# Kernel optimization log

Hardware: AMD Instinct MI355X
Metric: run time of the kernel (lower is better)

## Reference

```python
import jax, jax.numpy as jnp
import numpy as np

TEMP = 0.1
DROPOUT_PROB = 0.1
EPS = 1e-8  # torch F.cosine_similarity eps


def setup_inputs() -> dict:
    key = jax.random.key(0)
    k1, k2 = jax.random.split(key)
    N, D = 8192, 1024
    inputs = jax.random.normal(k1, (N, D), dtype=jnp.float32)
    noise = jax.random.uniform(k2, (N, D), dtype=jnp.float32)
    return {"inputs": inputs, "noise": noise}


def reference(inputs, noise):
    keep = 1.0 - DROPOUT_PROB
    # inverted dropout (torch nn.Dropout in train mode)
    mask = jnp.where(noise < keep, 1.0 / keep, 0.0).astype(inputs.dtype)
    enhanced = inputs * mask

    # cosine similarity = normalized matmul; norms clamped at EPS like torch
    na = jnp.maximum(jnp.linalg.norm(inputs, axis=-1, keepdims=True), EPS)
    nb = jnp.maximum(jnp.linalg.norm(enhanced, axis=-1, keepdims=True), EPS)
    a = inputs / na            # (N, D)
    b = enhanced / nb          # (N, D)
    logits = jnp.einsum('nd,md->nm', a, b) / TEMP  # (N, N)

    # cross-entropy with labels = arange(N), mean reduction
    lse = jax.nn.logsumexp(logits, axis=-1)          # (N,)
    diag = jnp.diagonal(logits)                      # (N,)
    return jnp.mean(lse - diag)
```

## Files before the change

kernel.cpp:

```cpp
#include <hip/hip_runtime.h>
#include <hip/hip_bf16.h>

#define N 8192
#define D 1024
#define BM 128
#define BN 256
#define BK 32
#define NKT (D / BK)

static constexpr float TEMP = 0.1f;
static constexpr float KEEP = 0.9f;
static constexpr float EPSN = 1e-8f;

typedef __attribute__((ext_vector_type(8))) short bf16x8;
typedef __attribute__((ext_vector_type(4))) float f32x4;

__device__ __forceinline__ void gload_lds16(const void* gsrc, void* ldst) {
  __builtin_amdgcn_global_load_lds(
      (const __attribute__((address_space(1))) void*)gsrc,
      (__attribute__((address_space(3))) void*)ldst, 16, 0, 0);
}

struct bf4pack { __hip_bfloat16 v[4]; };

__global__ __launch_bounds__(256) void UCR_prep(
    const float* __restrict__ inputs, const float* __restrict__ noise,
    __hip_bfloat16* __restrict__ aB, __hip_bfloat16* __restrict__ bB,
    float* __restrict__ diag, float* __restrict__ S, float* __restrict__ out)
{
  const int row = blockIdx.x;
  const int t = threadIdx.x;
  const float4 x = ((const float4*)(inputs + (size_t)row * D))[t];
  const float4 u = ((const float4*)(noise  + (size_t)row * D))[t];
  const float inv_keep = 1.0f / KEEP;
  float4 e;
  e.x = (u.x < KEEP) ? x.x * inv_keep : 0.0f;
  e.y = (u.y < KEEP) ? x.y * inv_keep : 0.0f;
  e.z = (u.z < KEEP) ? x.z * inv_keep : 0.0f;
  e.w = (u.w < KEEP) ? x.w * inv_keep : 0.0f;

  float sx  = x.x*x.x + x.y*x.y + x.z*x.z + x.w*x.w;
  float se  = e.x*e.x + e.y*e.y + e.z*e.z + e.w*e.w;
  float sxe = x.x*e.x + x.y*e.y + x.z*e.z + x.w*e.w;

  #pragma unroll
  for (int off = 1; off < 64; off <<= 1) {
    sx  += __shfl_xor(sx, off);
    se  += __shfl_xor(se, off);
    sxe += __shfl_xor(sxe, off);
  }
  __shared__ float red[3][4];
  const int wid = t >> 6, lane = t & 63;
  if (lane == 0) { red[0][wid] = sx; red[1][wid] = se; red[2][wid] = sxe; }
  __syncthreads();
  sx  = red[0][0] + red[0][1] + red[0][2] + red[0][3];
  se  = red[1][0] + red[1][1] + red[1][2] + red[1][3];
  sxe = red[2][0] + red[2][1] + red[2][2] + red[2][3];

  const float na = fmaxf(sqrtf(sx), EPSN);
  const float nb = fmaxf(sqrtf(se), EPSN);
  const float sa = 1.0f / (na * TEMP);
  const float sb = 1.0f / nb;
  if (t == 0) {
    diag[row] = sxe / (na * nb * TEMP);
    S[row] = 0.0f;
    if (row == 0) out[0] = 0.0f;
  }

  bf4pack pa, pb;
  pa.v[0] = __float2bfloat16(x.x * sa); pa.v[1] = __float2bfloat16(x.y * sa);
  pa.v[2] = __float2bfloat16(x.z * sa); pa.v[3] = __float2bfloat16(x.w * sa);
  pb.v[0] = __float2bfloat16(e.x * sb); pb.v[1] = __float2bfloat16(e.y * sb);
  pb.v[2] = __float2bfloat16(e.z * sb); pb.v[3] = __float2bfloat16(e.w * sb);
  ((bf4pack*)(aB + (size_t)row * D))[t] = pa;
  ((bf4pack*)(bB + (size_t)row * D))[t] = pb;
}

__global__ __launch_bounds__(256, 2) void UCR_gemm(
    const __hip_bfloat16* __restrict__ Aw, const __hip_bfloat16* __restrict__ Bw,
    float* __restrict__ S)
{
  __shared__ char lds[73728];

  const int t = threadIdx.x;
  const int lane = t & 63;
  const int wid = t >> 6;

  const int bid = blockIdx.x;
  const int u = bid >> 3;
  const int tm = (bid & 7) * 8 + (u & 7);
  const int tn = u >> 3;

  const char* Ag = (const char*)(Aw + (size_t)tm * BM * D);
  const char* Bg = (const char*)(Bw + (size_t)tn * BN * D);

  const char* aS[2]; const char* bS[4]; unsigned xA[2], xB[4];
  #pragma unroll
  for (int j = 0; j < 2; ++j) {
    const unsigned x = (unsigned)t * 16u + (unsigned)j * 4096u;
    const unsigned lin = x ^ (((x >> 7) & 3u) << 4);
    aS[j] = Ag + (size_t)(lin >> 6) * 2048 + (lin & 63u);
    xA[j] = x;
  }
  #pragma unroll
  for (int j = 0; j < 4; ++j) {
    const unsigned x = (unsigned)t * 16u + (unsigned)j * 4096u;
    const unsigned lin = x ^ (((x >> 7) & 3u) << 4);
    bS[j] = Bg + (size_t)(lin >> 6) * 2048 + (lin & 63u);
    xB[j] = x;
  }

#define STAGE(kt, L) do {                                   \
    gload_lds16(aS[0] + (kt) * 64, (L) + xA[0]);            \
    gload_lds16(aS[1] + (kt) * 64, (L) + xA[1]);            \
    gload_lds16(bS[0] + (kt) * 64, (L) + 8192 + xB[0]);     \
    gload_lds16(bS[1] + (kt) * 64, (L) + 8192 + xB[1]);     \
    gload_lds16(bS[2] + (kt) * 64, (L) + 8192 + xB[2]);     \
    gload_lds16(bS[3] + (kt) * 64, (L) + 8192 + xB[3]);     \
  } while (0)

  const int ln = lane & 15;
  const int cq = lane >> 4;
  const int colk = (cq * 16) ^ (((ln >> 1) & 3) << 4);
  const int aoff = ln * 64 + colk;
  const int boff = 8192 + wid * 4096 + ln * 64 + colk;

  f32x4 acc[8][4] = {};

  char* L0 = lds;
  char* L1 = lds + 24576;
  char* L2 = lds + 49152;

  STAGE(0, L0); STAGE(1, L1);
  asm volatile("s_waitcnt vmcnt(6)" ::: "memory");
  __builtin_amdgcn_s_barrier();

  for (int kt = 0; kt < NKT - 2; ++kt) {
    STAGE(kt + 2, L2);
    bf16x8 aF[8], bF[4];
    #pragma unroll
    for (int m = 0; m < 8; ++m)
      aF[m] = *(const bf16x8*)(L0 + m * 1024 + aoff);
    #pragma unroll
    for (int n = 0; n < 4; ++n)
      bF[n] = *(const bf16x8*)(L0 + n * 1024 + boff);
    __builtin_amdgcn_s_setprio(1);
    #pragma unroll
    for (int m = 0; m < 8; ++m)
      #pragma unroll
      for (int n = 0; n < 4; ++n)
        acc[m][n] = __builtin_amdgcn_mfma_f32_16x16x32_bf16(
            aF[m], bF[n], acc[m][n], 0, 0, 0);
    __builtin_amdgcn_s_setprio(0);
    asm volatile("s_waitcnt vmcnt(6)" ::: "memory");
    __builtin_amdgcn_s_barrier();
    char* tmp = L0; L0 = L1; L1 = L2; L2 = tmp;
  }
  {
    bf16x8 aF[8], bF[4];
    #pragma unroll
    for (int m = 0; m < 8; ++m)
      aF[m] = *(const bf16x8*)(L0 + m * 1024 + aoff);
    #pragma unroll
    for (int n = 0; n < 4; ++n)
      bF[n] = *(const bf16x8*)(L0 + n * 1024 + boff);
    __builtin_amdgcn_s_setprio(1);
    #pragma unroll
    for (int m = 0; m < 8; ++m)
      #pragma unroll
      for (int n = 0; n < 4; ++n)
        acc[m][n] = __builtin_amdgcn_mfma_f32_16x16x32_bf16(
            aF[m], bF[n], acc[m][n], 0, 0, 0);
    __builtin_amdgcn_s_setprio(0);
    asm volatile("s_waitcnt vmcnt(0)" ::: "memory");
    __builtin_amdgcn_s_barrier();
    char* tmp = L0; L0 = L1; L1 = L2; L2 = tmp;
  }
  {
    bf16x8 aF[8], bF[4];
    #pragma unroll
    for (int m = 0; m < 8; ++m)
      aF[m] = *(const bf16x8*)(L0 + m * 1024 + aoff);
    #pragma unroll
    for (int n = 0; n < 4; ++n)
      bF[n] = *(const bf16x8*)(L0 + n * 1024 + boff);
    #pragma unroll
    for (int m = 0; m < 8; ++m)
      #pragma unroll
      for (int n = 0; n < 4; ++n)
        acc[m][n] = __builtin_amdgcn_mfma_f32_16x16x32_bf16(
            aF[m], bF[n], acc[m][n], 0, 0, 0);
  }
#undef STAGE

  const int g = lane >> 4;
  const int c = lane & 15;
  const int rowbase = tm * BM;
  #pragma unroll
  for (int m = 0; m < 8; ++m) {
    #pragma unroll
    for (int i = 0; i < 4; ++i) {
      float s = 0.0f;
      #pragma unroll
      for (int n = 0; n < 4; ++n) s += __expf(acc[m][n][i]);
      #pragma unroll
      for (int off = 1; off < 16; off <<= 1) s += __shfl_xor(s, off);
      if (c == 0) atomicAdd(&S[rowbase + m * 16 + g * 4 + i], s);
    }
  }
}

__global__ __launch_bounds__(256) void UCR_loss(
    const float* __restrict__ S, const float* __restrict__ diag,
    float* __restrict__ out)
{
  const int i = blockIdx.x * 256 + threadIdx.x;
  float acc = logf(S[i]) - diag[i];
  #pragma unroll
  for (int off = 1; off < 64; off <<= 1) acc += __shfl_xor(acc, off);
  __shared__ float r[4];
  if ((threadIdx.x & 63) == 0) r[threadIdx.x >> 6] = acc;
  __syncthreads();
  if (threadIdx.x == 0)
    atomicAdd(out, (r[0] + r[1] + r[2] + r[3]) * (1.0f / (float)N));
}

extern "C" void kernel_launch(void* const* d_in, const int* in_sizes, int n_in,
                              void* d_out, int out_size, void* d_ws, size_t ws_size,
                              hipStream_t stream)
{
  const float* inputs = (const float*)d_in[0];
  const float* noise  = (const float*)d_in[1];

  char* ws = (char*)d_ws;
  __hip_bfloat16* aB = (__hip_bfloat16*)ws;
  __hip_bfloat16* bB = aB + (size_t)N * D;
  float* S    = (float*)(bB + (size_t)N * D);
  float* diag = S + N;

  UCR_prep<<<N, 256, 0, stream>>>(inputs, noise, aB, bB, diag, S, (float*)d_out);
  UCR_gemm<<<(N / BM) * (N / BN), 256, 0, stream>>>(aB, bB, S);
  UCR_loss<<<N / 256, 256, 0, stream>>>(S, diag, (float*)d_out);
}
```

Baseline: 246.7 us.

## Switch similarity GEMM from bf16 to scaled fp8 MFMA with exact diagonal

The prep kernel now quantizes the normalized, temperature-scaled operands to fp8 with fixed scale factors of 16 and 64, and the GEMM uses fp8 MFMA instructions with BK doubled to 64. This halves operand bytes and uses the higher-throughput fp8 matrix path. To limit the accuracy loss on the largest logit, diagonal tiles replace the quantized diagonal entry with the fp32 diag value before exponentiation. The risk is fp8 precision error in the logsumexp over the off-diagonal entries.

```diff
diff --git a/kernel.cpp b/kernel.cpp
--- a/kernel.cpp
+++ b/kernel.cpp
@@ -5,14 +5,14 @@
 #define D 1024
 #define BM 128
 #define BN 256
-#define BK 32
+#define BK 64
 #define NKT (D / BK)
 
 static constexpr float TEMP = 0.1f;
 static constexpr float KEEP = 0.9f;
 static constexpr float EPSN = 1e-8f;
-
-typedef __attribute__((ext_vector_type(8))) short bf16x8;
+static constexpr float INVS = 1.0f / 1024.0f;
+
 typedef __attribute__((ext_vector_type(4))) float f32x4;
 
 __device__ __forceinline__ void gload_lds16(const void* gsrc, void* ldst) {
@@ -21,11 +21,9 @@
       (__attribute__((address_space(3))) void*)ldst, 16, 0, 0);
 }
 
-struct bf4pack { __hip_bfloat16 v[4]; };
-
 __global__ __launch_bounds__(256) void UCR_prep(
     const float* __restrict__ inputs, const float* __restrict__ noise,
-    __hip_bfloat16* __restrict__ aB, __hip_bfloat16* __restrict__ bB,
+    unsigned char* __restrict__ a8, unsigned char* __restrict__ b8,
     float* __restrict__ diag, float* __restrict__ S, float* __restrict__ out)
 {
   const int row = blockIdx.x;
@@ -59,26 +57,25 @@
 
   const float na = fmaxf(sqrtf(sx), EPSN);
   const float nb = fmaxf(sqrtf(se), EPSN);
-  const float sa = 1.0f / (na * TEMP);
-  const float sb = 1.0f / nb;
+  const float sa = 16.0f / (na * TEMP);
+  const float sb = 64.0f / nb;
   if (t == 0) {
     diag[row] = sxe / (na * nb * TEMP);
     S[row] = 0.0f;
     if (row == 0) out[0] = 0.0f;
   }
 
-  bf4pack pa, pb;
-  pa.v[0] = __float2bfloat16(x.x * sa); pa.v[1] = __float2bfloat16(x.y * sa);
-  pa.v[2] = __float2bfloat16(x.z * sa); pa.v[3] = __float2bfloat16(x.w * sa);
-  pb.v[0] = __float2bfloat16(e.x * sb); pb.v[1] = __float2bfloat16(e.y * sb);
-  pb.v[2] = __float2bfloat16(e.z * sb); pb.v[3] = __float2bfloat16(e.w * sb);
-  ((bf4pack*)(aB + (size_t)row * D))[t] = pa;
-  ((bf4pack*)(bB + (size_t)row * D))[t] = pb;
+  int pa = __builtin_amdgcn_cvt_pk_fp8_f32(x.x * sa, x.y * sa, 0, false);
+  pa     = __builtin_amdgcn_cvt_pk_fp8_f32(x.z * sa, x.w * sa, pa, true);
+  int pb = __builtin_amdgcn_cvt_pk_fp8_f32(e.x * sb, e.y * sb, 0, false);
+  pb     = __builtin_amdgcn_cvt_pk_fp8_f32(e.z * sb, e.w * sb, pb, true);
+  ((int*)(a8 + (size_t)row * D))[t] = pa;
+  ((int*)(b8 + (size_t)row * D))[t] = pb;
 }
 
 __global__ __launch_bounds__(256, 2) void UCR_gemm(
-    const __hip_bfloat16* __restrict__ Aw, const __hip_bfloat16* __restrict__ Bw,
-    float* __restrict__ S)
+    const unsigned char* __restrict__ Aw, const unsigned char* __restrict__ Bw,
+    const float* __restrict__ diag, float* __restrict__ S)
 {
   __shared__ char lds[73728];
 
@@ -99,14 +96,14 @@
   for (int j = 0; j < 2; ++j) {
     const unsigned x = (unsigned)t * 16u + (unsigned)j * 4096u;
     const unsigned lin = x ^ (((x >> 7) & 3u) << 4);
-    aS[j] = Ag + (size_t)(lin >> 6) * 2048 + (lin & 63u);
+    aS[j] = Ag + (size_t)(lin >> 6) * D + (lin & 63u);
     xA[j] = x;
   }
   #pragma unroll
   for (int j = 0; j < 4; ++j) {
     const unsigned x = (unsigned)t * 16u + (unsigned)j * 4096u;
     const unsigned lin = x ^ (((x >> 7) & 3u) << 4);
-    bS[j] = Bg + (size_t)(lin >> 6) * 2048 + (lin & 63u);
+    bS[j] = Bg + (size_t)(lin >> 6) * D + (lin & 63u);
     xB[j] = x;
   }
 
@@ -121,9 +118,9 @@
 
   const int ln = lane & 15;
   const int cq = lane >> 4;
-  const int colk = (cq * 16) ^ (((ln >> 1) & 3) << 4);
-  const int aoff = ln * 64 + colk;
-  const int boff = 8192 + wid * 4096 + ln * 64 + colk;
+  const int offk0 = (cq * 8) ^ (((ln >> 1) & 3) << 4);
+  const int aoff = ln * 64 + offk0;
+  const int boff = 8192 + wid * 4096 + ln * 64 + offk0;
 
   f32x4 acc[8][4] = {};
 
@@ -137,75 +134,101 @@
 
   for (int kt = 0; kt < NKT - 2; ++kt) {
     STAGE(kt + 2, L2);
-    bf16x8 aF[8], bF[4];
-    #pragma unroll
-    for (int m = 0; m < 8; ++m)
-      aF[m] = *(const bf16x8*)(L0 + m * 1024 + aoff);
-    #pragma unroll
-    for (int n = 0; n < 4; ++n)
-      bF[n] = *(const bf16x8*)(L0 + n * 1024 + boff);
+    long aF[8][2], bF[4][2];
+    #pragma unroll
+    for (int m = 0; m < 8; ++m) {
+      aF[m][0] = *(const long*)(L0 + m * 1024 + aoff);
+      aF[m][1] = *(const long*)(L0 + m * 1024 + (aoff ^ 32));
+    }
+    #pragma unroll
+    for (int n = 0; n < 4; ++n) {
+      bF[n][0] = *(const long*)(L0 + n * 1024 + boff);
+      bF[n][1] = *(const long*)(L0 + n * 1024 + (boff ^ 32));
+    }
     __builtin_amdgcn_s_setprio(1);
     #pragma unroll
-    for (int m = 0; m < 8; ++m)
-      #pragma unroll
-      for (int n = 0; n < 4; ++n)
-        acc[m][n] = __builtin_amdgcn_mfma_f32_16x16x32_bf16(
-            aF[m], bF[n], acc[m][n], 0, 0, 0);
+    for (int ks = 0; ks < 2; ++ks)
+      #pragma unroll
+      for (int m = 0; m < 8; ++m)
+        #pragma unroll
+        for (int n = 0; n < 4; ++n)
+          acc[m][n] = __builtin_amdgcn_mfma_f32_16x16x32_fp8_fp8(
+              aF[m][ks], bF[n][ks], acc[m][n], 0, 0, 0);
     __builtin_amdgcn_s_setprio(0);
     asm volatile("s_waitcnt vmcnt(6)" ::: "memory");
     __builtin_amdgcn_s_barrier();
     char* tmp = L0; L0 = L1; L1 = L2; L2 = tmp;
   }
   {
-    bf16x8 aF[8], bF[4];
-    #pragma unroll
-    for (int m = 0; m < 8; ++m)
-      aF[m] = *(const bf16x8*)(L0 + m * 1024 + aoff);
-    #pragma unroll
-    for (int n = 0; n < 4; ++n)
-      bF[n] = *(const bf16x8*)(L0 + n * 1024 + boff);
+    long aF[8][2], bF[4][2];
+    #pragma unroll
+    for (int m = 0; m < 8; ++m) {
+      aF[m][0] = *(const long*)(L0 + m * 1024 + aoff);
+      aF[m][1] = *(const long*)(L0 + m * 1024 + (aoff ^ 32));
+    }
+    #pragma unroll
+    for (int n = 0; n < 4; ++n) {
+      bF[n][0] = *(const long*)(L0 + n * 1024 + boff);
+      bF[n][1] = *(const long*)(L0 + n * 1024 + (boff ^ 32));
+    }
     __builtin_amdgcn_s_setprio(1);
     #pragma unroll
-    for (int m = 0; m < 8; ++m)
-      #pragma unroll
-      for (int n = 0; n < 4; ++n)
-        acc[m][n] = __builtin_amdgcn_mfma_f32_16x16x32_bf16(
-            aF[m], bF[n], acc[m][n], 0, 0, 0);
+    for (int ks = 0; ks < 2; ++ks)
+      #pragma unroll
+      for (int m = 0; m < 8; ++m)
+        #pragma unroll
+        for (int n = 0; n < 4; ++n)
+          acc[m][n] = __builtin_amdgcn_mfma_f32_16x16x32_fp8_fp8(
+              aF[m][ks], bF[n][ks], acc[m][n], 0, 0, 0);
     __builtin_amdgcn_s_setprio(0);
     asm volatile("s_waitcnt vmcnt(0)" ::: "memory");
     __builtin_amdgcn_s_barrier();
     char* tmp = L0; L0 = L1; L1 = L2; L2 = tmp;
   }
   {
-    bf16x8 aF[8], bF[4];
-    #pragma unroll
-    for (int m = 0; m < 8; ++m)
-      aF[m] = *(const bf16x8*)(L0 + m * 1024 + aoff);
-    #pragma unroll
-    for (int n = 0; n < 4; ++n)
-      bF[n] = *(const bf16x8*)(L0 + n * 1024 + boff);
-    #pragma unroll
-    for (int m = 0; m < 8; ++m)
-      #pragma unroll
-      for (int n = 0; n < 4; ++n)
-        acc[m][n] = __builtin_amdgcn_mfma_f32_16x16x32_bf16(
-            aF[m], bF[n], acc[m][n], 0, 0, 0);
+    long aF[8][2], bF[4][2];
+    #pragma unroll
+    for (int m = 0; m < 8; ++m) {
+      aF[m][0] = *(const long*)(L0 + m * 1024 + aoff);
+      aF[m][1] = *(const long*)(L0 + m * 1024 + (aoff ^ 32));
+    }
+    #pragma unroll
+    for (int n = 0; n < 4; ++n) {
+      bF[n][0] = *(const long*)(L0 + n * 1024 + boff);
+      bF[n][1] = *(const long*)(L0 + n * 1024 + (boff ^ 32));
+    }
+    #pragma unroll
+    for (int ks = 0; ks < 2; ++ks)
+      #pragma unroll
+      for (int m = 0; m < 8; ++m)
+        #pragma unroll
+        for (int n = 0; n < 4; ++n)
+          acc[m][n] = __builtin_amdgcn_mfma_f32_16x16x32_fp8_fp8(
+              aF[m][ks], bF[n][ks], acc[m][n], 0, 0, 0);
   }
 #undef STAGE
 
   const int g = lane >> 4;
-  const int c = lane & 15;
+  const int cc = lane & 15;
   const int rowbase = tm * BM;
+  const int colb = tn * BN + wid * 64;
+  const bool hasdiag = (tn == (tm >> 1));
   #pragma unroll
   for (int m = 0; m < 8; ++m) {
     #pragma unroll
     for (int i = 0; i < 4; ++i) {
+      const int row = rowbase + m * 16 + g * 4 + i;
+      const float dv = hasdiag ? diag[row] : 0.0f;
       float s = 0.0f;
       #pragma unroll
-      for (int n = 0; n < 4; ++n) s += __expf(acc[m][n][i]);
+      for (int n = 0; n < 4; ++n) {
+        float v = acc[m][n][i] * INVS;
+        if (hasdiag && (colb + n * 16 + cc) == row) v = dv;
+        s += __expf(v);
+      }
       #pragma unroll
       for (int off = 1; off < 16; off <<= 1) s += __shfl_xor(s, off);
-      if (c == 0) atomicAdd(&S[rowbase + m * 16 + g * 4 + i], s);
+      if (cc == 0) atomicAdd(&S[row], s);
     }
   }
 }
@@ -233,12 +256,12 @@
   const float* noise  = (const float*)d_in[1];
 
   char* ws = (char*)d_ws;
-  __hip_bfloat16* aB = (__hip_bfloat16*)ws;
-  __hip_bfloat16* bB = aB + (size_t)N * D;
-  float* S    = (float*)(bB + (size_t)N * D);
+  unsigned char* a8 = (unsigned char*)ws;
+  unsigned char* b8 = a8 + (size_t)N * D;
+  float* S    = (float*)(b8 + (size_t)N * D);
   float* diag = S + N;
 
-  UCR_prep<<<N, 256, 0, stream>>>(inputs, noise, aB, bB, diag, S, (float*)d_out);
-  UCR_gemm<<<(N / BM) * (N / BN), 256, 0, stream>>>(aB, bB, S);
+  UCR_prep<<<N, 256, 0, stream>>>(inputs, noise, a8, b8, diag, S, (float*)d_out);
+  UCR_gemm<<<(N / BM) * (N / BN), 256, 0, stream>>>(a8, b8, diag, S);
   UCR_loss<<<N / 256, 256, 0, stream>>>(S, diag, (float*)d_out);
 }
```

Result: no change. 244.1 us (-1.1%).
